# Kernel tuning notes

Hardware: AMD Instinct MI355X
Metric: run time of the kernel (lower is better)

The kernel has to match this reference:

```python
import jax, jax.numpy as jnp
import numpy as np

# ---- Cl(4,1) geometric-product Cayley table: gp(a,b)[k] = a[i] b[j] C[i,j,k] ----
def _build_cayley():
    metric = np.array([1.0, 1.0, 1.0, 1.0, -1.0], dtype=np.float32)  # signature (4,1)
    C = np.zeros((32, 32, 32), dtype=np.float32)
    for a in range(32):
        for b in range(32):
            # canonical reordering sign (count of swaps to merge blades)
            cnt = 0
            ash = a >> 1
            while ash:
                cnt += bin(ash & b).count('1')
                ash >>= 1
            s = -1.0 if (cnt & 1) else 1.0
            common = a & b
            for i in range(5):
                if (common >> i) & 1:
                    s *= metric[i]
            C[a, b, a ^ b] = s
    return C

CAYLEY = _build_cayley()
N_HEADS = 8

def gp_cl41(a, b, C):
    # a, b: (..., 32) multivectors
    return jnp.einsum('...i,...j,ijk->...k', a, b, C)

def normalize_cl41(x, eps=1e-6):
    n = jnp.sqrt(jnp.sum(x * x, axis=-1, keepdims=True) + eps)
    return x / n

def vlinear(x, w, b):
    # x: (..., Din, 32), w: (Dout, Din), b: (Dout, 32) -- blade-wise channel mixing
    return jnp.einsum('...ik,oi->...ok', x, w) + b

def layernorm2d(x, w, b, eps=1e-5):
    # normalized_shape = [D, 32]
    m = jnp.mean(x, axis=(-2, -1), keepdims=True)
    v = jnp.var(x, axis=(-2, -1), keepdims=True)
    return (x - m) / jnp.sqrt(v + eps) * w + b

def attention(x, wq, bq, wk, bk, wv, bv, wo, bo):
    B, S, D, K = x.shape
    hd = D // N_HEADS
    q = vlinear(x, wq, bq).reshape(B, S, N_HEADS, hd, K)
    k = vlinear(x, wk, bk).reshape(B, S, N_HEADS, hd, K)
    v = vlinear(x, wv, bv).reshape(B, S, N_HEADS, hd, K)
    scores = jnp.einsum('bqhdk,bshdk->bhqs', q, k) / jnp.sqrt(jnp.float32(hd * K))
    p = jax.nn.softmax(scores, axis=-1)
    o = jnp.einsum('bhqs,bshdk->bqhdk', p, v).reshape(B, S, D, K)
    return vlinear(o, wo, bo)


def setup_inputs() -> dict:
    key = jax.random.key(0)
    B, S, D, K = 4, 512, 256, 32
    L, E, NC = 2, 4, 1000
    ks = jax.random.split(key, 24)
    s = 1.0 / np.sqrt(D)
    inp = {
        'x': jax.random.normal(ks[0], (B, S, D, K), jnp.float32),
        'ln1_w': jnp.ones((L, D, K), jnp.float32),
        'ln1_b': jnp.zeros((L, D, K), jnp.float32),
        'wq': jax.random.normal(ks[1], (L, D, D), jnp.float32) * s,
        'bq': jnp.zeros((L, D, K), jnp.float32),
        'wk': jax.random.normal(ks[2], (L, D, D), jnp.float32) * s,
        'bk': jnp.zeros((L, D, K), jnp.float32),
        'wv': jax.random.normal(ks[3], (L, D, D), jnp.float32) * s,
        'bv': jnp.zeros((L, D, K), jnp.float32),
        'wo': jax.random.normal(ks[4], (L, D, D), jnp.float32) * s,
        'bo': jnp.zeros((L, D, K), jnp.float32),
        'ln2_w': jnp.ones((L, D, K), jnp.float32),
        'ln2_b': jnp.zeros((L, D, K), jnp.float32),
        'w1': jax.random.normal(ks[5], (L, E * D, D), jnp.float32) * s,
        'b1': jnp.zeros((L, E * D, K), jnp.float32),
        'w2': jax.random.normal(ks[6], (L, D, E * D), jnp.float32) * (1.0 / np.sqrt(E * D)),
        'b2': jnp.zeros((L, D, K), jnp.float32),
        'wr': jax.random.normal(ks[7], (D, D), jnp.float32) * s,
        'br': jnp.zeros((D, K), jnp.float32),
        'wc': jax.random.normal(ks[8], (NC, D * K), jnp.float32) * 0.02,
        'bc': jnp.zeros((NC,), jnp.float32),
    }
    return inp


def reference(x, ln1_w, ln1_b, wq, bq, wk, bk, wv, bv, wo, bo,
              ln2_w, ln2_b, w1, b1, w2, b2, wr, br, wc, bc):
    C = jnp.asarray(CAYLEY)
    L = ln1_w.shape[0]
    for l in range(L):
        h = layernorm2d(x, ln1_w[l], ln1_b[l])
        x = x + attention(h, wq[l], bq[l], wk[l], bk[l], wv[l], bv[l], wo[l], bo[l])
        x = normalize_cl41(x)
        h = layernorm2d(x, ln2_w[l], ln2_b[l])
        h = jnp.tanh(vlinear(h, w1[l], b1[l]))
        x = x + vlinear(h, w2[l], b2[l])
        x = normalize_cl41(x)
    # Recursive Rotor Accumulator pooling: psi_{t+1} = normalize(gp(r_t, psi_t))
    delta = vlinear(x, wr, br)                    # (B, S, D, 32)
    B, S, D, K = delta.shape
    psi0 = jnp.zeros((B, D, K), x.dtype).at[..., 0].set(1.0)
    def step(psi, r_t):
        return normalize_cl41(gp_cl41(r_t, psi, C)), None
    psi, _ = jax.lax.scan(step, psi0, jnp.moveaxis(delta, 1, 0))
    logits = psi.reshape(B, D * K) @ wc.T + bc
    return logits
```

## Files before the change

kernel.cpp:

```cpp
#include <hip/hip_runtime.h>
#include <hip/hip_bf16.h>
#include <cstdint>
#include <cstddef>

typedef __bf16 bf16_t;
typedef __attribute__((ext_vector_type(8))) __bf16 bf16x8;
typedef __attribute__((ext_vector_type(4))) __bf16 bf16x4;
typedef __attribute__((ext_vector_type(4))) float f32x4;

#define DEV __device__ __forceinline__

DEV void async16(const bf16_t* g, bf16_t* l) {
  __builtin_amdgcn_global_load_lds((const __attribute__((address_space(1))) void*)g,
                                   (__attribute__((address_space(3))) void*)l, 16, 0, 0);
}

DEV float fast_tanh(float x) {
  const float ex = __expf(2.f * x);
  return 1.f - 2.f / (ex + 1.f);
}

enum { EPI_RESID = 0, EPI_FFN1 = 1, EPI_QKV = 2, EPI_SCORE = 3, EPI_PV = 4, EPI_DELTAT = 5 };

template<int EPI, bool TRANSB>
__global__ __launch_bounds__(256, 2)
void gemm_k(const bf16_t* __restrict__ A, const bf16_t* __restrict__ A2,
            const bf16_t* __restrict__ B, const bf16_t* __restrict__ B2,
            const float* __restrict__ bias, void* __restrict__ outp, void* __restrict__ outp2,
            int Kd, int lda, int ldb, long aStride, long bStride)
{
  __shared__ bf16_t sA [2][4096];
  __shared__ bf16_t sB [2][4096];
  __shared__ bf16_t sA2[2][4096];
  __shared__ bf16_t sB2[2][4096];

  const int tid  = threadIdx.x;
  const int lane = tid & 63;
  const int wv   = tid >> 6;
  const int wr   = wv >> 1, wc = wv & 1;

  unsigned gx = gridDim.x, gy = gridDim.y;
  unsigned nb = gx * gy * gridDim.z;
  unsigned fid = blockIdx.x + gx * (blockIdx.y + gy * blockIdx.z);
  if ((nb & 7u) == 0u) fid = (fid & 7u) * (nb >> 3) + (fid >> 3);
  const unsigned bxu = fid % gx;
  const unsigned rem = fid / gx;
  const unsigned byu = rem % gy;
  const unsigned bzu = rem / gy;
  const int m0 = byu * 128;
  const int n0 = bxu * 128;
  const int bz = bzu;

  const bf16_t *Ab, *Bb, *A2b, *B2b;
  if constexpr (EPI == EPI_SCORE) {
    const int h = bz & 7;
    const long ho = (long)(bz >> 3) * 512;
    Ab  = A  + (long)h * aStride + ho;
    Bb  = B  + (long)h * bStride + ho;
    A2b = A2 + (long)h * aStride + ho;
    B2b = B2 + (long)h * bStride + ho;
  } else {
    Ab  = A  + (long)bz * aStride;
    Bb  = B  + (long)bz * bStride;
    A2b = A2 + (long)bz * aStride;
    B2b = B2 + (long)bz * bStride;
  }

  const int sRow = tid >> 2;
  const int sKo  = (tid & 3) * 8;
  const int tr = tid & 15;
  const int tc = tid >> 4;

  f32x4 acc[4][4];
#pragma unroll
  for (int i = 0; i < 4; i++)
#pragma unroll
    for (int j = 0; j < 4; j++) acc[i][j] = f32x4{0.f, 0.f, 0.f, 0.f};

  const int ns  = Kd >> 5;
  const int off = (int)(fid & (unsigned)(ns - 1));

  uint4 br0, br1, br2, br3;

  auto stageA = [&](int si, int b) {
    const int kt = ((si + off) & (ns - 1)) << 5;
    const bf16_t* ga  = Ab  + (long)(m0 + sRow) * lda + kt + sKo;
    const bf16_t* ga2 = A2b + (long)(m0 + sRow) * lda + kt + sKo;
    async16(ga,             &sA [b][tid * 8]);
    async16(ga + 64 * lda,  &sA [b][2048 + tid * 8]);
    async16(ga2,            &sA2[b][tid * 8]);
    async16(ga2 + 64 * lda, &sA2[b][2048 + tid * 8]);
  };
  auto stageB = [&](int si, int b) {
    const int kt = ((si + off) & (ns - 1)) << 5;
    const bf16_t* gb  = Bb  + (long)(n0 + sRow) * ldb + kt + sKo;
    const bf16_t* gb2 = B2b + (long)(n0 + sRow) * ldb + kt + sKo;
    async16(gb,             &sB [b][tid * 8]);
    async16(gb + 64 * ldb,  &sB [b][2048 + tid * 8]);
    async16(gb2,            &sB2[b][tid * 8]);
    async16(gb2 + 64 * ldb, &sB2[b][2048 + tid * 8]);
  };
  auto loadBR = [&](int si) {
    const int kt = ((si + off) & (ns - 1)) << 5;
    const bf16_t* gb  = Bb  + (long)(kt + tr) * ldb + n0 + tc * 8;
    const bf16_t* gb2 = B2b + (long)(kt + tr) * ldb + n0 + tc * 8;
    br0 = *(const uint4*)gb;
    br1 = *(const uint4*)(gb + 16 * ldb);
    br2 = *(const uint4*)gb2;
    br3 = *(const uint4*)(gb2 + 16 * ldb);
  };

  stageA(0, 0);
  if constexpr (!TRANSB) stageB(0, 0); else loadBR(0);

  for (int si = 0; si < ns; si++) {
    const int cb = si & 1;
    if (si + 1 < ns) stageA(si + 1, cb ^ 1);
    if constexpr (TRANSB) {
      const bf16_t* e0 = (const bf16_t*)&br0;
      const bf16_t* e1 = (const bf16_t*)&br1;
      const bf16_t* e2 = (const bf16_t*)&br2;
      const bf16_t* e3 = (const bf16_t*)&br3;
#pragma unroll
      for (int j = 0; j < 8; j++) {
        sB [cb][(tc * 8 + j) * 32 + tr]      = e0[j];
        sB [cb][(tc * 8 + j) * 32 + tr + 16] = e1[j];
        sB2[cb][(tc * 8 + j) * 32 + tr]      = e2[j];
        sB2[cb][(tc * 8 + j) * 32 + tr + 16] = e3[j];
      }
      if (si + 1 < ns) loadBR(si + 1);
      if (si + 1 >= ns) asm volatile("s_waitcnt vmcnt(0)" ::: "memory");
    } else {
      if (si + 1 < ns) {
        stageB(si + 1, cb ^ 1);
        asm volatile("s_waitcnt vmcnt(8)" ::: "memory");
      } else {
        asm volatile("s_waitcnt vmcnt(0)" ::: "memory");
      }
    }
    __syncthreads();

    bf16x8 af[4], bfr[4], af2[4], bf2[4];
#pragma unroll
    for (int i = 0; i < 4; i++) {
      const int ao = (wr * 64 + i * 16 + (lane & 15)) * 32 + (lane >> 4) * 8;
      const int bo = (wc * 64 + i * 16 + (lane & 15)) * 32 + (lane >> 4) * 8;
      af[i]  = *(const bf16x8*)&sA [cb][ao];
      af2[i] = *(const bf16x8*)&sA2[cb][ao];
      bfr[i] = *(const bf16x8*)&sB [cb][bo];
      bf2[i] = *(const bf16x8*)&sB2[cb][bo];
    }
#pragma unroll
    for (int i = 0; i < 4; i++)
#pragma unroll
      for (int j = 0; j < 4; j++) {
        acc[i][j] = __builtin_amdgcn_mfma_f32_16x16x32_bf16(af[i],  bfr[j], acc[i][j], 0, 0, 0);
        acc[i][j] = __builtin_amdgcn_mfma_f32_16x16x32_bf16(af[i],  bf2[j], acc[i][j], 0, 0, 0);
        acc[i][j] = __builtin_amdgcn_mfma_f32_16x16x32_bf16(af2[i], bfr[j], acc[i][j], 0, 0, 0);
      }
    __syncthreads();
  }

  const int cn = lane & 15;
  const int rg = (lane >> 4) * 4;
#pragma unroll
  for (int i = 0; i < 4; i++) {
    const int mb = m0 + wr * 64 + i * 16 + rg;
#pragma unroll
    for (int j = 0; j < 4; j++) {
      const int n = n0 + wc * 64 + j * 16 + cn;
#pragma unroll
      for (int r = 0; r < 4; r++) {
        const int m = mb + r;
        const float v = acc[i][j][r];
        if constexpr (EPI == EPI_RESID) {
          const float bb = bias ? bias[n * 32 + (m & 31)] : 0.f;
          ((float*)outp)[(long)m * 256 + n] += v + bb;
        } else if constexpr (EPI == EPI_QKV) {
          const int s = m >> 5, kb = m & 31;
          const int proj = n >> 8, col = n & 255;
          const int h = col >> 5, dd = col & 31;
          const long oidx = (long)proj * 4194304 + (long)(h * 512 + s) * 1024 + kb * 32 + dd;
          const float t = v + bias[n * 32 + kb];
          const bf16_t hh = (bf16_t)t;
          ((bf16_t*)outp)[oidx]  = hh;
          ((bf16_t*)outp2)[oidx] = (bf16_t)(t - (float)hh);
        } else if constexpr (EPI == EPI_SCORE) {
          const int h = bz & 7, half = bz >> 3;
          float* dst = half ? (float*)outp2 : (float*)outp;
          dst[(long)h * 262144 + (long)m * 512 + n] = v * (1.f / 32.f);
        } else if constexpr (EPI == EPI_PV) {
          const int kb = n >> 5, dd = n & 31;
          const long oidx = (long)(m * 32 + kb) * 256 + bz * 32 + dd;
          const bf16_t hh = (bf16_t)v;
          ((bf16_t*)outp)[oidx]  = hh;
          ((bf16_t*)outp2)[oidx] = (bf16_t)(v - (float)hh);
        } else {
          const int b = m >> 14, t = (m >> 5) & 511, kb = m & 31;
          ((float*)outp)[(((long)(b * 256 + n) * 512 + t) * 32) + kb] = v + bias[n * 32 + kb];
        }
      }
    }
  }
}

__global__ __launch_bounds__(512, 1)
void ffn_k(const bf16_t* __restrict__ Ah, const bf16_t* __restrict__ Al,
           const bf16_t* __restrict__ W1h_, const bf16_t* __restrict__ W1l_,
           const bf16_t* __restrict__ W2h_, const bf16_t* __restrict__ W2l_,
           const float* __restrict__ b1, const float* __restrict__ b2,
           float* __restrict__ XT)
{
  __shared__ bf16_t sAh[64 * 256], sAl[64 * 256];
  __shared__ bf16_t sWh[8192], sWl[8192];
  __shared__ bf16_t sHh[64 * 136], sHl[64 * 136];

  const int tid  = threadIdx.x;
  const int lane = tid & 63;
  const int wv   = tid >> 6;
  const int wm   = wv >> 2;
  const int wn   = wv & 3;
  const int l15  = lane & 15;
  const int lg   = lane >> 4;
  const int m0   = blockIdx.x * 64;
  const int coff = blockIdx.x & 7;
  const int soff = (blockIdx.x >> 3) & 7;
  const int toff = (blockIdx.x >> 3) & 3;

#pragma unroll
  for (int r = 0; r < 4; r++) {
    const int idx = r * 512 + tid;
    const int row = idx >> 5, cp = idx & 31;
    const int c = cp ^ (row & 31);
    async16(Ah + (long)(m0 + row) * 256 + c * 8, sAh + idx * 8);
    async16(Al + (long)(m0 + row) * 256 + c * 8, sAl + idx * 8);
  }
  asm volatile("s_waitcnt vmcnt(0)" ::: "memory");
  __syncthreads();

  f32x4 acc2[2][4];
#pragma unroll
  for (int i = 0; i < 2; i++)
#pragma unroll
    for (int j = 0; j < 4; j++) acc2[i][j] = f32x4{0.f, 0.f, 0.f, 0.f};

  const int wrow = tid >> 2;
  const int wc1  = (tid & 3) ^ (wrow & 3);

#pragma unroll 1
  for (int cc = 0; cc < 8; cc++) {
    const int ch = (cc + coff) & 7;
    const bf16_t* W1h = W1h_ + (long)(ch * 128) * 256;
    const bf16_t* W1l = W1l_ + (long)(ch * 128) * 256;
    async16(W1h + (long)wrow * 256 + soff * 32 + wc1 * 8, sWh + tid * 8);
    async16(W1l + (long)wrow * 256 + soff * 32 + wc1 * 8, sWl + tid * 8);

    f32x4 acc1[2][2];
#pragma unroll
    for (int i = 0; i < 2; i++)
#pragma unroll
      for (int j = 0; j < 2; j++) acc1[i][j] = f32x4{0.f, 0.f, 0.f, 0.f};

    for (int s = 0; s < 8; s++) {
      const int cb = (s & 1) * 4096;
      const int sp = (s + soff) & 7;
      if (s < 7) {
        const int nbuf = ((s + 1) & 1) * 4096;
        const int spn = (s + 1 + soff) & 7;
        async16(W1h + (long)wrow * 256 + spn * 32 + wc1 * 8, sWh + nbuf + tid * 8);
        async16(W1l + (long)wrow * 256 + spn * 32 + wc1 * 8, sWl + nbuf + tid * 8);
        asm volatile("s_waitcnt vmcnt(2)" ::: "memory");
      } else {
        asm volatile("s_waitcnt vmcnt(0)" ::: "memory");
      }
      __syncthreads();
      bf16x8 a_h[2], a_l[2], w_h[2], w_l[2];
#pragma unroll
      for (int i = 0; i < 2; i++) {
        const int arow = wm * 32 + i * 16 + l15;
        const int ac = (sp * 4 + lg) ^ (arow & 31);
        a_h[i] = *(const bf16x8*)&sAh[arow * 256 + ac * 8];
        a_l[i] = *(const bf16x8*)&sAl[arow * 256 + ac * 8];
      }
#pragma unroll
      for (int j = 0; j < 2; j++) {
        const int nrow = wn * 32 + j * 16 + l15;
        const int ncp = lg ^ (nrow & 3);
        w_h[j] = *(const bf16x8*)&sWh[cb + nrow * 32 + ncp * 8];
        w_l[j] = *(const bf16x8*)&sWl[cb + nrow * 32 + ncp * 8];
      }
#pragma unroll
      for (int i = 0; i < 2; i++)
#pragma unroll
        for (int j = 0; j < 2; j++) {
          acc1[i][j] = __builtin_amdgcn_mfma_f32_16x16x32_bf16(w_h[j], a_h[i], acc1[i][j], 0, 0, 0);
          acc1[i][j] = __builtin_amdgcn_mfma_f32_16x16x32_bf16(w_h[j], a_l[i], acc1[i][j], 0, 0, 0);
          acc1[i][j] = __builtin_amdgcn_mfma_f32_16x16x32_bf16(w_l[j], a_h[i], acc1[i][j], 0, 0, 0);
        }
      __syncthreads();
    }

    uint4 wrg_h[2], wrg_l[2];
#pragma unroll
    for (int r = 0; r < 2; r++) {
      const int idx = r * 512 + tid;
      const int row = idx >> 2;
      const int c = (idx & 3) ^ (row & 3);
      wrg_h[r] = *(const uint4*)(W2h_ + (long)row * 1024 + ch * 128 + toff * 32 + c * 8);
      wrg_l[r] = *(const uint4*)(W2l_ + (long)row * 1024 + ch * 128 + toff * 32 + c * 8);
    }

#pragma unroll
    for (int i = 0; i < 2; i++) {
      const int m = wm * 32 + i * 16 + l15;
      const int kb = (m0 + m) & 31;
#pragma unroll
      for (int j = 0; j < 2; j++) {
        const int nb4 = wn * 32 + j * 16 + lg * 4;
        bf16x4 h4, l4;
#pragma unroll
        for (int rr = 0; rr < 4; rr++) {
          const int n = nb4 + rr;
          const float t = fast_tanh(acc1[i][j][rr] + b1[(ch * 128 + n) * 32 + kb]);
          const bf16_t hh = (bf16_t)t;
          h4[rr] = hh;
          l4[rr] = (bf16_t)(t - (float)hh);
        }
        *(bf16x4*)&sHh[m * 136 + nb4] = h4;
        *(bf16x4*)&sHl[m * 136 + nb4] = l4;
      }
    }
    __syncthreads();

    for (int t = 0; t < 4; t++) {
      const int tp = (t + toff) & 3;
#pragma unroll
      for (int r = 0; r < 2; r++) {
        const int idx = r * 512 + tid;
        *(uint4*)&sWh[idx * 8] = wrg_h[r];
        *(uint4*)&sWl[idx * 8] = wrg_l[r];
      }
      __syncthreads();
      if (t < 3) {
        const int tpn = (t + 1 + toff) & 3;
#pragma unroll
        for (int r = 0; r < 2; r++) {
          const int idx = r * 512 + tid;
          const int row = idx >> 2;
          const int c = (idx & 3) ^ (row & 3);
          wrg_h[r] = *(const uint4*)(W2h_ + (long)row * 1024 + ch * 128 + tpn * 32 + c * 8);
          wrg_l[r] = *(const uint4*)(W2l_ + (long)row * 1024 + ch * 128 + tpn * 32 + c * 8);
        }
      }
      bf16x8 h_h[2], h_l[2], v_h[4], v_l[4];
#pragma unroll
      for (int i = 0; i < 2; i++) {
        const int hrow = wm * 32 + i * 16 + l15;
        h_h[i] = *(const bf16x8*)&sHh[hrow * 136 + tp * 32 + lg * 8];
        h_l[i] = *(const bf16x8*)&sHl[hrow * 136 + tp * 32 + lg * 8];
      }
#pragma unroll
      for (int j = 0; j < 4; j++) {
        const int n2 = wn * 64 + j * 16 + l15;
        const int ncp = lg ^ (n2 & 3);
        v_h[j] = *(const bf16x8*)&sWh[n2 * 32 + ncp * 8];
        v_l[j] = *(const bf16x8*)&sWl[n2 * 32 + ncp * 8];
      }
#pragma unroll
      for (int i = 0; i < 2; i++)
#pragma unroll
        for (int j = 0; j < 4; j++) {
          acc2[i][j] = __builtin_amdgcn_mfma_f32_16x16x32_bf16(h_h[i], v_h[j], acc2[i][j], 0, 0, 0);
          acc2[i][j] = __builtin_amdgcn_mfma_f32_16x16x32_bf16(h_h[i], v_l[j], acc2[i][j], 0, 0, 0);
          acc2[i][j] = __builtin_amdgcn_mfma_f32_16x16x32_bf16(h_l[i], v_h[j], acc2[i][j], 0, 0, 0);
        }
      __syncthreads();
    }
  }

#pragma unroll
  for (int i = 0; i < 2; i++)
#pragma unroll
    for (int j = 0; j < 4; j++) {
      const int n2 = wn * 64 + j * 16 + l15;
#pragma unroll
      for (int rr = 0; rr < 4; rr++) {
        const int m = m0 + wm * 32 + i * 16 + lg * 4 + rr;
        XT[(long)m * 256 + n2] += acc2[i][j][rr] + b2[n2 * 32 + (m & 31)];
      }
    }
}

__global__ __launch_bounds__(256)
void transpose_k(const float* __restrict__ src, float* __restrict__ dst, int R, int C)
{
  __shared__ float t[32][33];
  const long boff = (long)blockIdx.z * R * C;
  const int r0 = blockIdx.y * 32, c0 = blockIdx.x * 32;
  const int tx = threadIdx.x & 31, ty = threadIdx.x >> 5;
#pragma unroll
  for (int i = 0; i < 32; i += 8)
    t[ty + i][tx] = src[boff + (long)(r0 + ty + i) * C + c0 + tx];
  __syncthreads();
#pragma unroll
  for (int i = 0; i < 32; i += 8)
    dst[boff + (long)(c0 + ty + i) * R + r0 + tx] = t[tx][ty + i];
}

DEV void hilo4(const f32x4 t, bf16x4& h, bf16x4& l) {
#pragma unroll
  for (int j = 0; j < 4; j++) {
    const bf16_t hh = (bf16_t)t[j];
    h[j] = hh;
    l[j] = (bf16_t)(t[j] - (float)hh);
  }
}

template<int MODE>
__global__ __launch_bounds__(256)
void nl_k(const float* __restrict__ X, float* __restrict__ Xo,
          const float* __restrict__ wT, const float* __restrict__ bT,
          bf16_t* __restrict__ oh, bf16_t* __restrict__ ol)
{
  const int row = blockIdx.x * 4 + (threadIdx.x >> 6);
  const int l   = threadIdx.x & 63;
  const float4* Xr = (const float4*)X + (long)row * 2048 + l;
  f32x4 v[32];
#pragma unroll
  for (int kb = 0; kb < 32; kb++) {
    const float4 t = Xr[kb * 64];
    v[kb] = f32x4{t.x, t.y, t.z, t.w};
  }
  if constexpr (MODE & 1) {
    f32x4 ss = f32x4{1e-6f, 1e-6f, 1e-6f, 1e-6f};
#pragma unroll
    for (int kb = 0; kb < 32; kb++) ss += v[kb] * v[kb];
    const f32x4 rs = f32x4{rsqrtf(ss[0]), rsqrtf(ss[1]), rsqrtf(ss[2]), rsqrtf(ss[3])};
#pragma unroll
    for (int kb = 0; kb < 32; kb++) v[kb] *= rs;
    if constexpr (MODE & 2) {
      float4* Xw = (float4*)Xo + (long)row * 2048 + l;
#pragma unroll
      for (int kb = 0; kb < 32; kb++)
        Xw[kb * 64] = float4{v[kb][0], v[kb][1], v[kb][2], v[kb][3]};
    }
  }
  if constexpr (MODE & 4) {
    float s = 0.f, s2 = 0.f;
#pragma unroll
    for (int kb = 0; kb < 32; kb++) {
      s  += (v[kb][0] + v[kb][1]) + (v[kb][2] + v[kb][3]);
      s2 += (v[kb][0] * v[kb][0] + v[kb][1] * v[kb][1]) +
            (v[kb][2] * v[kb][2] + v[kb][3] * v[kb][3]);
    }
#pragma unroll
    for (int o = 32; o > 0; o >>= 1) { s += __shfl_xor(s, o); s2 += __shfl_xor(s2, o); }
    const float mean = s * (1.f / 8192.f);
    const float var  = s2 * (1.f / 8192.f) - mean * mean;
    const float rstd = rsqrtf(var + 1e-5f);
    const float4* w4 = (const float4*)wT + l;
    const float4* b4 = (const float4*)bT + l;
#pragma unroll
    for (int kb = 0; kb < 32; kb++) {
      const float4 ww = w4[kb * 64];
      const float4 bb = b4[kb * 64];
      f32x4 t;
      t[0] = (v[kb][0] - mean) * rstd * ww.x + bb.x;
      t[1] = (v[kb][1] - mean) * rstd * ww.y + bb.y;
      t[2] = (v[kb][2] - mean) * rstd * ww.z + bb.z;
      t[3] = (v[kb][3] - mean) * rstd * ww.w + bb.w;
      bf16x4 h4, l4;
      hilo4(t, h4, l4);
      const long oi = (long)row * 8192 + kb * 256 + l * 4;
      *(bf16x4*)&oh[oi] = h4;
      *(bf16x4*)&ol[oi] = l4;
    }
  }
  if constexpr (MODE & 8) {
#pragma unroll
    for (int kb = 0; kb < 32; kb++) {
      bf16x4 h4, l4;
      hilo4(v[kb], h4, l4);
      const long oi = (long)row * 8192 + kb * 256 + l * 4;
      *(bf16x4*)&oh[oi] = h4;
      *(bf16x4*)&ol[oi] = l4;
    }
  }
}

__global__ __launch_bounds__(256)
void softmax_k(const float* __restrict__ SC, const float* __restrict__ SC2,
               bf16_t* __restrict__ Ph, bf16_t* __restrict__ Pl)
{
  const int row = blockIdx.x * 4 + (threadIdx.x >> 6);
  const int lane = threadIdx.x & 63;
  const float* s1 = SC  + (long)row * 512;
  const float* s2 = SC2 + (long)row * 512;
  float4 a = *(const float4*)&s1[lane * 4];
  float4 c = *(const float4*)&s1[256 + lane * 4];
  const float4 a2 = *(const float4*)&s2[lane * 4];
  const float4 c2 = *(const float4*)&s2[256 + lane * 4];
  a.x += a2.x; a.y += a2.y; a.z += a2.z; a.w += a2.w;
  c.x += c2.x; c.y += c2.y; c.z += c2.z; c.w += c2.w;
  float mx = fmaxf(fmaxf(fmaxf(a.x, a.y), fmaxf(a.z, a.w)),
                   fmaxf(fmaxf(c.x, c.y), fmaxf(c.z, c.w)));
#pragma unroll
  for (int o = 32; o > 0; o >>= 1) mx = fmaxf(mx, __shfl_xor(mx, o));
  float e[8] = {expf(a.x - mx), expf(a.y - mx), expf(a.z - mx), expf(a.w - mx),
                expf(c.x - mx), expf(c.y - mx), expf(c.z - mx), expf(c.w - mx)};
  float sum = ((e[0] + e[1]) + (e[2] + e[3])) + ((e[4] + e[5]) + (e[6] + e[7]));
#pragma unroll
  for (int o = 32; o > 0; o >>= 1) sum += __shfl_xor(sum, o);
  const float inv = 1.f / sum;
  bf16x4 h0, h1, l0, l1;
#pragma unroll
  for (int j = 0; j < 4; j++) {
    const float p0 = e[j] * inv, p1 = e[4 + j] * inv;
    h0[j] = (bf16_t)p0; l0[j] = (bf16_t)(p0 - (float)h0[j]);
    h1[j] = (bf16_t)p1; l1[j] = (bf16_t)(p1 - (float)h1[j]);
  }
  *(bf16x4*)&Ph[(long)row * 512 + lane * 4] = h0;
  *(bf16x4*)&Ph[(long)row * 512 + 256 + lane * 4] = h1;
  *(bf16x4*)&Pl[(long)row * 512 + lane * 4] = l0;
  *(bf16x4*)&Pl[(long)row * 512 + 256 + lane * 4] = l1;
}

constexpr float gpsign(int i, int j) {
  int cnt = 0;
  for (int s = 1; s < 5; s++) cnt += __builtin_popcount((i >> s) & j);
  float sgn = (cnt & 1) ? -1.f : 1.f;
  if ((i & j) & 16) sgn = -sgn;
  return sgn;
}

DEV void gp32(const float* __restrict__ a, const float* __restrict__ b, float* __restrict__ o) {
#pragma unroll
  for (int k = 0; k < 32; k++) {
    float s0 = 0.f, s1 = 0.f;
#pragma unroll
    for (int i = 0; i < 32; i += 2) {
      s0 = fmaf(gpsign(i, i ^ k) * a[i], b[i ^ k], s0);
      s1 = fmaf(gpsign(i + 1, (i + 1) ^ k) * a[i + 1], b[(i + 1) ^ k], s1);
    }
    o[k] = s0 + s1;
  }
}

__global__ __launch_bounds__(256)
void gptree_k(const float* __restrict__ dT, float* __restrict__ psiO)
{
  __shared__ float bufA[256 * 33];
  __shared__ float bufB[128 * 33];
  const int chain = blockIdx.x;
  const int t = threadIdx.x;
  const float* src = dT + (long)chain * (512 * 32);
  {
    float v[64];
    const float4* g = (const float4*)(src + t * 64);
#pragma unroll
    for (int i = 0; i < 16; i++) *(float4*)&v[i * 4] = g[i];
    float o[32];
    gp32(v + 32, v, o);
    float ss = 1e-6f;
#pragma unroll
    for (int k = 0; k < 32; k++) ss = fmaf(o[k], o[k], ss);
    const float rs = rsqrtf(ss);
#pragma unroll
    for (int k = 0; k < 32; k++) bufA[t * 33 + k] = o[k] * rs;
  }
  __syncthreads();
  int cur = 0;
#pragma unroll 1
  for (int P = 128; P >= 1; P >>= 1) {
    const float* in = cur ? bufB : bufA;
    float* ob = cur ? bufA : bufB;
    if (t < P) {
      float a[32], b[32], o[32];
#pragma unroll
      for (int c = 0; c < 32; c++) { b[c] = in[t * 66 + c]; a[c] = in[t * 66 + 33 + c]; }
      gp32(a, b, o);
      float ss = 1e-6f;
#pragma unroll
      for (int k = 0; k < 32; k++) ss = fmaf(o[k], o[k], ss);
      const float rs = rsqrtf(ss);
#pragma unroll
      for (int k = 0; k < 32; k++) ob[t * 33 + k] = o[k] * rs;
    }
    cur ^= 1;
    __syncthreads();
  }
  if (t < 32) psiO[(long)chain * 32 + t] = (cur ? bufB : bufA)[t];
}

__global__ __launch_bounds__(256)
void cls_k(const float* __restrict__ psi, const float* __restrict__ wcw,
           const float* __restrict__ bc, float* __restrict__ out)
{
  const int c = blockIdx.x;
  const int tid = threadIdx.x;
  float a0 = 0.f, a1 = 0.f, a2 = 0.f, a3 = 0.f;
  for (int i = tid * 4; i < 8192; i += 1024) {
    const float4 w  = *(const float4*)&wcw[(long)c * 8192 + i];
    const float4 p0 = *(const float4*)&psi[i];
    const float4 p1 = *(const float4*)&psi[8192 + i];
    const float4 p2 = *(const float4*)&psi[16384 + i];
    const float4 p3 = *(const float4*)&psi[24576 + i];
    a0 += w.x * p0.x + w.y * p0.y + w.z * p0.z + w.w * p0.w;
    a1 += w.x * p1.x + w.y * p1.y + w.z * p1.z + w.w * p1.w;
    a2 += w.x * p2.x + w.y * p2.y + w.z * p2.z + w.w * p2.w;
    a3 += w.x * p3.x + w.y * p3.y + w.z * p3.z + w.w * p3.w;
  }
#pragma unroll
  for (int o = 32; o > 0; o >>= 1) {
    a0 += __shfl_down(a0, o); a1 += __shfl_down(a1, o);
    a2 += __shfl_down(a2, o); a3 += __shfl_down(a3, o);
  }
  __shared__ float red[4][4];
  const int wv = tid >> 6;
  if ((tid & 63) == 0) { red[wv][0] = a0; red[wv][1] = a1; red[wv][2] = a2; red[wv][3] = a3; }
  __syncthreads();
  if (tid < 4) {
    const float r = red[0][tid] + red[1][tid] + red[2][tid] + red[3][tid] + bc[c];
    out[(long)tid * 1000 + c] = r;
  }
}

__global__ void split_k(const float* __restrict__ in, bf16_t* __restrict__ h,
                        bf16_t* __restrict__ l, int n)
{
  const int i = blockIdx.x * 256 + threadIdx.x;
  if (i < n) {
    const float v = in[i];
    const bf16_t hh = (bf16_t)v;
    h[i] = hh;
    l[i] = (bf16_t)(v - (float)hh);
  }
}

__global__ void cpy_k(const float* __restrict__ in, float* __restrict__ o, int n)
{
  const int i = blockIdx.x * 256 + threadIdx.x;
  if (i < n) o[i] = in[i];
}

extern "C" void kernel_launch(void* const* d_in, const int* in_sizes, int n_in,
                              void* d_out, int out_size, void* d_ws, size_t ws_size,
                              hipStream_t stream)
{
  const float* x    = (const float*)d_in[0];
  const float* ln1w = (const float*)d_in[1];
  const float* ln1b = (const float*)d_in[2];
  const float* wq   = (const float*)d_in[3];
  const float* bq   = (const float*)d_in[4];
  const float* wk   = (const float*)d_in[5];
  const float* bk   = (const float*)d_in[6];
  const float* wvv  = (const float*)d_in[7];
  const float* bv   = (const float*)d_in[8];
  const float* wo   = (const float*)d_in[9];
  const float* bo   = (const float*)d_in[10];
  const float* ln2w = (const float*)d_in[11];
  const float* ln2b = (const float*)d_in[12];
  const float* w1   = (const float*)d_in[13];
  const float* b1   = (const float*)d_in[14];
  const float* w2   = (const float*)d_in[15];
  const float* b2   = (const float*)d_in[16];
  const float* wr   = (const float*)d_in[17];
  const float* br   = (const float*)d_in[18];
  const float* wcw  = (const float*)d_in[19];
  const float* bc   = (const float*)d_in[20];
  float* out = (float*)d_out;

  char* ws = (char*)d_ws;
  const size_t MB = 1ull << 20;
  const size_t KB = 1024;
  float*  XT   = (float*)(ws + 0);
  bf16_t* HBh  = (bf16_t*)(ws + 64 * MB);
  bf16_t* HBl  = (bf16_t*)(ws + 96 * MB);
  bf16_t* QKVh = (bf16_t*)(ws + 128 * MB);
  bf16_t* QKVl = (bf16_t*)(ws + 152 * MB);
  float*  SCb  = (float*)(ws + 176 * MB);
  float*  SC2b = (float*)(ws + 184 * MB);
  bf16_t* Ph   = QKVh;
  bf16_t* Pl   = QKVl;
  bf16_t* OBh  = QKVh + 4194304;
  bf16_t* OBl  = QKVl + 4194304;
  bf16_t* Vh   = QKVh + 8388608;
  bf16_t* Vl   = QKVl + 8388608;
  bf16_t* XHI = (bf16_t*)(ws + 64 * MB), *XLO = (bf16_t*)(ws + 96 * MB);
  float*  DELTAT = (float*)(ws + 128 * MB);
  float*  PSI  = (float*)(ws + 192 * MB);
  char*   W    = ws + 193 * MB;
  bf16_t* WQKVh = (bf16_t*)(W);
  bf16_t* WQKVl = (bf16_t*)(W + 1 * MB);
  bf16_t* W1h = (bf16_t*)(W + 2 * MB);   bf16_t* W1l = (bf16_t*)(W + 3 * MB);
  bf16_t* W2h = (bf16_t*)(W + 4 * MB);   bf16_t* W2l = (bf16_t*)(W + 5 * MB);
  bf16_t* WOh = (bf16_t*)(W + 6 * MB);   bf16_t* WOl = (bf16_t*)(W + 6 * MB + 256 * KB);
  bf16_t* WRh = (bf16_t*)(W + 6 * MB + 512 * KB);
  bf16_t* WRl = (bf16_t*)(W + 6 * MB + 640 * KB);
  float*  BQKV = (float*)(W + 6 * MB + 768 * KB);
  float*  LNT  = (float*)(W + 6 * MB + 960 * KB);
  float* LN1WT = LNT, *LN1BT = LNT + 16384, *LN2WT = LNT + 32768, *LN2BT = LNT + 49152;

  for (int l = 0; l < 2; l++) {
    split_k<<<256, 256, 0, stream>>>(wq + l * 65536, WQKVh + l * 196608, WQKVl + l * 196608, 65536);
    split_k<<<256, 256, 0, stream>>>(wk + l * 65536, WQKVh + l * 196608 + 65536, WQKVl + l * 196608 + 65536, 65536);
    split_k<<<256, 256, 0, stream>>>(wvv + l * 65536, WQKVh + l * 196608 + 131072, WQKVl + l * 196608 + 131072, 65536);
    cpy_k<<<32, 256, 0, stream>>>(bq + l * 8192, BQKV + l * 24576, 8192);
    cpy_k<<<32, 256, 0, stream>>>(bk + l * 8192, BQKV + l * 24576 + 8192, 8192);
    cpy_k<<<32, 256, 0, stream>>>(bv + l * 8192, BQKV + l * 24576 + 16384, 8192);
  }
  split_k<<<512, 256, 0, stream>>>(wo, WOh, WOl, 131072);
  split_k<<<2048, 256, 0, stream>>>(w1, W1h, W1l, 524288);
  split_k<<<2048, 256, 0, stream>>>(w2, W2h, W2l, 524288);
  split_k<<<256, 256, 0, stream>>>(wr, WRh, WRl, 65536);
  transpose_k<<<dim3(1, 8, 2), 256, 0, stream>>>(ln1w, LN1WT, 256, 32);
  transpose_k<<<dim3(1, 8, 2), 256, 0, stream>>>(ln1b, LN1BT, 256, 32);
  transpose_k<<<dim3(1, 8, 2), 256, 0, stream>>>(ln2w, LN2WT, 256, 32);
  transpose_k<<<dim3(1, 8, 2), 256, 0, stream>>>(ln2b, LN2BT, 256, 32);

  transpose_k<<<dim3(1, 8, 2048), 256, 0, stream>>>(x, XT, 256, 32);

  for (int l = 0; l < 2; l++) {
    if (l == 0)
      nl_k<4><<<512, 256, 0, stream>>>(XT, nullptr, LN1WT, LN1BT, HBh, HBl);
    for (int b = 0; b < 4; b++) {
      const long ao = (long)b * 16384 * 256;
      gemm_k<EPI_QKV, false><<<dim3(6, 128, 1), 256, 0, stream>>>(
          HBh + ao, HBl + ao, WQKVh + l * 196608, WQKVl + l * 196608,
          BQKV + l * 24576, QKVh, QKVl, 256, 256, 256, 0, 0);
      gemm_k<EPI_SCORE, false><<<dim3(4, 4, 16), 256, 0, stream>>>(
          QKVh, QKVl, QKVh + 4194304, QKVl + 4194304,
          nullptr, SCb, SC2b, 512, 1024, 1024, 512 * 1024, 512 * 1024);
      softmax_k<<<1024, 256, 0, stream>>>(SCb, SC2b, Ph, Pl);
      gemm_k<EPI_PV, true><<<dim3(8, 4, 8), 256, 0, stream>>>(
          Ph, Pl, Vh, Vl, nullptr, OBh, OBl, 512, 512, 1024, 512 * 512, 512 * 1024);
      gemm_k<EPI_RESID, false><<<dim3(2, 128, 1), 256, 0, stream>>>(
          OBh, OBl, WOh + l * 65536, WOl + l * 65536,
          bo + l * 8192, (float*)XT + ao, nullptr, 256, 256, 256, 0, 0);
    }
    nl_k<1 | 2 | 4><<<512, 256, 0, stream>>>(XT, XT, LN2WT + l * 8192, LN2BT + l * 8192, HBh, HBl);
    ffn_k<<<1024, 512, 0, stream>>>(HBh, HBl,
                                    W1h + l * 262144, W1l + l * 262144,
                                    W2h + l * 262144, W2l + l * 262144,
                                    b1 + l * 32768, b2 + l * 8192, XT);
    if (l == 0) {
      nl_k<1 | 2 | 4><<<512, 256, 0, stream>>>(XT, XT, LN1WT + 8192, LN1BT + 8192, HBh, HBl);
    } else {
      nl_k<1 | 8><<<512, 256, 0, stream>>>(XT, nullptr, nullptr, nullptr, XHI, XLO);
    }
  }

  gemm_k<EPI_DELTAT, false><<<dim3(2, 512, 1), 256, 0, stream>>>(
      XHI, XLO, WRh, WRl, br, DELTAT, nullptr, 256, 256, 256, 0, 0);
  gptree_k<<<1024, 256, 0, stream>>>(DELTAT, PSI);
  cls_k<<<1000, 256, 0, stream>>>(PSI, wcw, bc, out);
}
```

Measured before the change: 2.158 ms.

## Halve FFN row tile to 32 rows for two blocks per CU

The fused FFN kernel now processes 32 rows per block instead of 64, doubling the grid and roughly halving LDS and accumulator registers so two 512-thread blocks can be resident per CU. The hidden-activation buffer drops its padded stride of 136 in favour of an XOR-swizzled stride of 128 to avoid bank conflicts while saving LDS. In exchange, each block reuses every loaded W1/W2 tile across only half as many rows, which doubles the weight traffic from L2 and lowers the MFMA count per sync.

```diff
diff --git a/kernel.cpp b/kernel.cpp
--- a/kernel.cpp
+++ b/kernel.cpp
@@ -204,16 +204,16 @@
   }
 }
 
-__global__ __launch_bounds__(512, 1)
+__global__ __launch_bounds__(512, 2)
 void ffn_k(const bf16_t* __restrict__ Ah, const bf16_t* __restrict__ Al,
            const bf16_t* __restrict__ W1h_, const bf16_t* __restrict__ W1l_,
            const bf16_t* __restrict__ W2h_, const bf16_t* __restrict__ W2l_,
            const float* __restrict__ b1, const float* __restrict__ b2,
            float* __restrict__ XT)
 {
-  __shared__ bf16_t sAh[64 * 256], sAl[64 * 256];
+  __shared__ bf16_t sAh[32 * 256], sAl[32 * 256];
   __shared__ bf16_t sWh[8192], sWl[8192];
-  __shared__ bf16_t sHh[64 * 136], sHl[64 * 136];
+  __shared__ bf16_t sHh[32 * 128], sHl[32 * 128];
 
   const int tid  = threadIdx.x;
   const int lane = tid & 63;
@@ -222,13 +222,13 @@
   const int wn   = wv & 3;
   const int l15  = lane & 15;
   const int lg   = lane >> 4;
-  const int m0   = blockIdx.x * 64;
+  const int m0   = blockIdx.x * 32;
   const int coff = blockIdx.x & 7;
   const int soff = (blockIdx.x >> 3) & 7;
   const int toff = (blockIdx.x >> 3) & 3;
 
 #pragma unroll
-  for (int r = 0; r < 4; r++) {
+  for (int r = 0; r < 2; r++) {
     const int idx = r * 512 + tid;
     const int row = idx >> 5, cp = idx & 31;
     const int c = cp ^ (row & 31);
@@ -238,11 +238,9 @@
   asm volatile("s_waitcnt vmcnt(0)" ::: "memory");
   __syncthreads();
 
-  f32x4 acc2[2][4];
-#pragma unroll
-  for (int i = 0; i < 2; i++)
-#pragma unroll
-    for (int j = 0; j < 4; j++) acc2[i][j] = f32x4{0.f, 0.f, 0.f, 0.f};
+  f32x4 acc2[4];
+#pragma unroll
+  for (int j = 0; j < 4; j++) acc2[j] = f32x4{0.f, 0.f, 0.f, 0.f};
 
   const int wrow = tid >> 2;
   const int wc1  = (tid & 3) ^ (wrow & 3);
@@ -255,11 +253,9 @@
     async16(W1h + (long)wrow * 256 + soff * 32 + wc1 * 8, sWh + tid * 8);
     async16(W1l + (long)wrow * 256 + soff * 32 + wc1 * 8, sWl + tid * 8);
 
-    f32x4 acc1[2][2];
-#pragma unroll
-    for (int i = 0; i < 2; i++)
-#pragma unroll
-      for (int j = 0; j < 2; j++) acc1[i][j] = f32x4{0.f, 0.f, 0.f, 0.f};
+    f32x4 acc1[2];
+#pragma unroll
+    for (int j = 0; j < 2; j++) acc1[j] = f32x4{0.f, 0.f, 0.f, 0.f};
 
     for (int s = 0; s < 8; s++) {
       const int cb = (s & 1) * 4096;
@@ -274,13 +270,12 @@
         asm volatile("s_waitcnt vmcnt(0)" ::: "memory");
       }
       __syncthreads();
-      bf16x8 a_h[2], a_l[2], w_h[2], w_l[2];
-#pragma unroll
-      for (int i = 0; i < 2; i++) {
-        const int arow = wm * 32 + i * 16 + l15;
+      bf16x8 a_h, a_l, w_h[2], w_l[2];
+      {
+        const int arow = wm * 16 + l15;
         const int ac = (sp * 4 + lg) ^ (arow & 31);
-        a_h[i] = *(const bf16x8*)&sAh[arow * 256 + ac * 8];
-        a_l[i] = *(const bf16x8*)&sAl[arow * 256 + ac * 8];
+        a_h = *(const bf16x8*)&sAh[arow * 256 + ac * 8];
+        a_l = *(const bf16x8*)&sAl[arow * 256 + ac * 8];
       }
 #pragma unroll
       for (int j = 0; j < 2; j++) {
@@ -290,13 +285,11 @@
         w_l[j] = *(const bf16x8*)&sWl[cb + nrow * 32 + ncp * 8];
       }
 #pragma unroll
-      for (int i = 0; i < 2; i++)
-#pragma unroll
-        for (int j = 0; j < 2; j++) {
-          acc1[i][j] = __builtin_amdgcn_mfma_f32_16x16x32_bf16(w_h[j], a_h[i], acc1[i][j], 0, 0, 0);
-          acc1[i][j] = __builtin_amdgcn_mfma_f32_16x16x32_bf16(w_h[j], a_l[i], acc1[i][j], 0, 0, 0);
-          acc1[i][j] = __builtin_amdgcn_mfma_f32_16x16x32_bf16(w_l[j], a_h[i], acc1[i][j], 0, 0, 0);
-        }
+      for (int j = 0; j < 2; j++) {
+        acc1[j] = __builtin_amdgcn_mfma_f32_16x16x32_bf16(w_h[j], a_h, acc1[j], 0, 0, 0);
+        acc1[j] = __builtin_amdgcn_mfma_f32_16x16x32_bf16(w_h[j], a_l, acc1[j], 0, 0, 0);
+        acc1[j] = __builtin_amdgcn_mfma_f32_16x16x32_bf16(w_l[j], a_h, acc1[j], 0, 0, 0);
+      }
       __syncthreads();
     }
 
@@ -310,24 +303,25 @@
       wrg_l[r] = *(const uint4*)(W2l_ + (long)row * 1024 + ch * 128 + toff * 32 + c * 8);
     }
 
-#pragma unroll
-    for (int i = 0; i < 2; i++) {
-      const int m = wm * 32 + i * 16 + l15;
+    {
+      const int m = wm * 16 + l15;
       const int kb = (m0 + m) & 31;
 #pragma unroll
       for (int j = 0; j < 2; j++) {
-        const int nb4 = wn * 32 + j * 16 + lg * 4;
+        const int u = wn * 4 + j * 2 + (lg >> 1);
+        const int pu = u ^ (m & 7);
+        const int base = m * 128 + pu * 8 + (lg & 1) * 4;
+        const int ncol = wn * 32 + j * 16 + lg * 4;
         bf16x4 h4, l4;
 #pragma unroll
         for (int rr = 0; rr < 4; rr++) {
-          const int n = nb4 + rr;
-          const float t = fast_tanh(acc1[i][j][rr] + b1[(ch * 128 + n) * 32 + kb]);
+          const float t = fast_tanh(acc1[j][rr] + b1[(ch * 128 + ncol + rr) * 32 + kb]);
           const bf16_t hh = (bf16_t)t;
           h4[rr] = hh;
           l4[rr] = (bf16_t)(t - (float)hh);
         }
-        *(bf16x4*)&sHh[m * 136 + nb4] = h4;
-        *(bf16x4*)&sHl[m * 136 + nb4] = l4;
+        *(bf16x4*)&sHh[base] = h4;
+        *(bf16x4*)&sHl[base] = l4;
       }
     }
     __syncthreads();
@@ -352,12 +346,12 @@
           wrg_l[r] = *(const uint4*)(W2l_ + (long)row * 1024 + ch * 128 + tpn * 32 + c * 8);
         }
       }
-      bf16x8 h_h[2], h_l[2], v_h[4], v_l[4];
-#pragma unroll
-      for (int i = 0; i < 2; i++) {
-        const int hrow = wm * 32 + i * 16 + l15;
-        h_h[i] = *(const bf16x8*)&sHh[hrow * 136 + tp * 32 + lg * 8];
-        h_l[i] = *(const bf16x8*)&sHl[hrow * 136 + tp * 32 + lg * 8];
+      bf16x8 h_h, h_l, v_h[4], v_l[4];
+      {
+        const int hrow = wm * 16 + l15;
+        const int pu = (tp * 4 + lg) ^ (hrow & 7);
+        h_h = *(const bf16x8*)&sHh[hrow * 128 + pu * 8];
+        h_l = *(const bf16x8*)&sHl[hrow * 128 + pu * 8];
       }
 #pragma unroll
       for (int j = 0; j < 4; j++) {
@@ -367,28 +361,24 @@
         v_l[j] = *(const bf16x8*)&sWl[n2 * 32 + ncp * 8];
       }
 #pragma unroll
-      for (int i = 0; i < 2; i++)
-#pragma unroll
-        for (int j = 0; j < 4; j++) {
-          acc2[i][j] = __builtin_amdgcn_mfma_f32_16x16x32_bf16(h_h[i], v_h[j], acc2[i][j], 0, 0, 0);
-          acc2[i][j] = __builtin_amdgcn_mfma_f32_16x16x32_bf16(h_h[i], v_l[j], acc2[i][j], 0, 0, 0);
-          acc2[i][j] = __builtin_amdgcn_mfma_f32_16x16x32_bf16(h_l[i], v_h[j], acc2[i][j], 0, 0, 0);
-        }
+      for (int j = 0; j < 4; j++) {
+        acc2[j] = __builtin_amdgcn_mfma_f32_16x16x32_bf16(h_h, v_h[j], acc2[j], 0, 0, 0);
+        acc2[j] = __builtin_amdgcn_mfma_f32_16x16x32_bf16(h_h, v_l[j], acc2[j], 0, 0, 0);
+        acc2[j] = __builtin_amdgcn_mfma_f32_16x16x32_bf16(h_l, v_h[j], acc2[j], 0, 0, 0);
+      }
       __syncthreads();
     }
   }
 
 #pragma unroll
-  for (int i = 0; i < 2; i++)
-#pragma unroll
-    for (int j = 0; j < 4; j++) {
-      const int n2 = wn * 64 + j * 16 + l15;
-#pragma unroll
-      for (int rr = 0; rr < 4; rr++) {
-        const int m = m0 + wm * 32 + i * 16 + lg * 4 + rr;
-        XT[(long)m * 256 + n2] += acc2[i][j][rr] + b2[n2 * 32 + (m & 31)];
-      }
-    }
+  for (int j = 0; j < 4; j++) {
+    const int n2 = wn * 64 + j * 16 + l15;
+#pragma unroll
+    for (int rr = 0; rr < 4; rr++) {
+      const int m = m0 + wm * 16 + lg * 4 + rr;
+      XT[(long)m * 256 + n2] += acc2[j][rr] + b2[n2 * 32 + (m & 31)];
+    }
+  }
 }
 
 __global__ __launch_bounds__(256)
@@ -739,7 +729,7 @@
           bo + l * 8192, (float*)XT + ao, nullptr, 256, 256, 256, 0, 0);
     }
     nl_k<1 | 2 | 4><<<512, 256, 0, stream>>>(XT, XT, LN2WT + l * 8192, LN2BT + l * 8192, HBh, HBl);
-    ffn_k<<<1024, 512, 0, stream>>>(HBh, HBl,
+    ffn_k<<<2048, 512, 0, stream>>>(HBh, HBl,
                                     W1h + l * 262144, W1l + l * 262144,
                                     W2h + l * 262144, W2l + l * 262144,
                                     b1 + l * 32768, b2 + l * 8192, XT);
```

Result: slower. 2.830 ms (+31.1%).

## Shrink FFN tile to 32 rows and read weights directly from global

Applied to the files above, without the earlier changes.

The fused FFN kernel now uses 256-thread blocks covering 32 rows each, launched as 2048 blocks with two blocks per CU. The LDS staging and double buffering of W1 and W2 tiles, with their barriers, are removed. Each wave now loads its weight fragments straight from global memory, relying on L1/L2 caching. This cuts LDS use and synchronisation and may raise occupancy, but weight traffic per row of output doubles, and the uncoalesced per-lane global loads sit right before the MFMAs with no prefetch to hide their latency.

```diff
diff --git a/kernel.cpp b/kernel.cpp
--- a/kernel.cpp
+++ b/kernel.cpp
@@ -204,32 +204,29 @@
   }
 }
 
-__global__ __launch_bounds__(512, 1)
+__global__ __launch_bounds__(256, 2)
 void ffn_k(const bf16_t* __restrict__ Ah, const bf16_t* __restrict__ Al,
            const bf16_t* __restrict__ W1h_, const bf16_t* __restrict__ W1l_,
            const bf16_t* __restrict__ W2h_, const bf16_t* __restrict__ W2l_,
            const float* __restrict__ b1, const float* __restrict__ b2,
            float* __restrict__ XT)
 {
-  __shared__ bf16_t sAh[64 * 256], sAl[64 * 256];
-  __shared__ bf16_t sWh[8192], sWl[8192];
-  __shared__ bf16_t sHh[64 * 136], sHl[64 * 136];
+  __shared__ bf16_t sAh[32 * 256], sAl[32 * 256];
+  __shared__ bf16_t sHh[32 * 136], sHl[32 * 136];
 
   const int tid  = threadIdx.x;
   const int lane = tid & 63;
-  const int wv   = tid >> 6;
-  const int wm   = wv >> 2;
-  const int wn   = wv & 3;
+  const int wn   = tid >> 6;
   const int l15  = lane & 15;
   const int lg   = lane >> 4;
-  const int m0   = blockIdx.x * 64;
+  const int m0   = blockIdx.x * 32;
   const int coff = blockIdx.x & 7;
   const int soff = (blockIdx.x >> 3) & 7;
   const int toff = (blockIdx.x >> 3) & 3;
 
 #pragma unroll
   for (int r = 0; r < 4; r++) {
-    const int idx = r * 512 + tid;
+    const int idx = r * 256 + tid;
     const int row = idx >> 5, cp = idx & 31;
     const int c = cp ^ (row & 31);
     async16(Ah + (long)(m0 + row) * 256 + c * 8, sAh + idx * 8);
@@ -243,17 +240,12 @@
   for (int i = 0; i < 2; i++)
 #pragma unroll
     for (int j = 0; j < 4; j++) acc2[i][j] = f32x4{0.f, 0.f, 0.f, 0.f};
-
-  const int wrow = tid >> 2;
-  const int wc1  = (tid & 3) ^ (wrow & 3);
 
 #pragma unroll 1
   for (int cc = 0; cc < 8; cc++) {
     const int ch = (cc + coff) & 7;
     const bf16_t* W1h = W1h_ + (long)(ch * 128) * 256;
     const bf16_t* W1l = W1l_ + (long)(ch * 128) * 256;
-    async16(W1h + (long)wrow * 256 + soff * 32 + wc1 * 8, sWh + tid * 8);
-    async16(W1l + (long)wrow * 256 + soff * 32 + wc1 * 8, sWl + tid * 8);
 
     f32x4 acc1[2][2];
 #pragma unroll
@@ -261,23 +253,13 @@
 #pragma unroll
       for (int j = 0; j < 2; j++) acc1[i][j] = f32x4{0.f, 0.f, 0.f, 0.f};
 
+#pragma unroll 2
     for (int s = 0; s < 8; s++) {
-      const int cb = (s & 1) * 4096;
       const int sp = (s + soff) & 7;
-      if (s < 7) {
-        const int nbuf = ((s + 1) & 1) * 4096;
-        const int spn = (s + 1 + soff) & 7;
-        async16(W1h + (long)wrow * 256 + spn * 32 + wc1 * 8, sWh + nbuf + tid * 8);
-        async16(W1l + (long)wrow * 256 + spn * 32 + wc1 * 8, sWl + nbuf + tid * 8);
-        asm volatile("s_waitcnt vmcnt(2)" ::: "memory");
-      } else {
-        asm volatile("s_waitcnt vmcnt(0)" ::: "memory");
-      }
-      __syncthreads();
       bf16x8 a_h[2], a_l[2], w_h[2], w_l[2];
 #pragma unroll
       for (int i = 0; i < 2; i++) {
-        const int arow = wm * 32 + i * 16 + l15;
+        const int arow = i * 16 + l15;
         const int ac = (sp * 4 + lg) ^ (arow & 31);
         a_h[i] = *(const bf16x8*)&sAh[arow * 256 + ac * 8];
         a_l[i] = *(const bf16x8*)&sAl[arow * 256 + ac * 8];
@@ -285,9 +267,8 @@
 #pragma unroll
       for (int j = 0; j < 2; j++) {
         const int nrow = wn * 32 + j * 16 + l15;
-        const int ncp = lg ^ (nrow & 3);
-        w_h[j] = *(const bf16x8*)&sWh[cb + nrow * 32 + ncp * 8];
-        w_l[j] = *(const bf16x8*)&sWl[cb + nrow * 32 + ncp * 8];
+        w_h[j] = *(const bf16x8*)(W1h + (long)nrow * 256 + sp * 32 + lg * 8);
+        w_l[j] = *(const bf16x8*)(W1l + (long)nrow * 256 + sp * 32 + lg * 8);
       }
 #pragma unroll
       for (int i = 0; i < 2; i++)
@@ -297,22 +278,11 @@
           acc1[i][j] = __builtin_amdgcn_mfma_f32_16x16x32_bf16(w_h[j], a_l[i], acc1[i][j], 0, 0, 0);
           acc1[i][j] = __builtin_amdgcn_mfma_f32_16x16x32_bf16(w_l[j], a_h[i], acc1[i][j], 0, 0, 0);
         }
-      __syncthreads();
-    }
-
-    uint4 wrg_h[2], wrg_l[2];
-#pragma unroll
-    for (int r = 0; r < 2; r++) {
-      const int idx = r * 512 + tid;
-      const int row = idx >> 2;
-      const int c = (idx & 3) ^ (row & 3);
-      wrg_h[r] = *(const uint4*)(W2h_ + (long)row * 1024 + ch * 128 + toff * 32 + c * 8);
-      wrg_l[r] = *(const uint4*)(W2l_ + (long)row * 1024 + ch * 128 + toff * 32 + c * 8);
     }
 
 #pragma unroll
     for (int i = 0; i < 2; i++) {
-      const int m = wm * 32 + i * 16 + l15;
+      const int m = i * 16 + l15;
       const int kb = (m0 + m) & 31;
 #pragma unroll
       for (int j = 0; j < 2; j++) {
@@ -332,39 +302,21 @@
     }
     __syncthreads();
 
+#pragma unroll 2
     for (int t = 0; t < 4; t++) {
       const int tp = (t + toff) & 3;
-#pragma unroll
-      for (int r = 0; r < 2; r++) {
-        const int idx = r * 512 + tid;
-        *(uint4*)&sWh[idx * 8] = wrg_h[r];
-        *(uint4*)&sWl[idx * 8] = wrg_l[r];
-      }
-      __syncthreads();
-      if (t < 3) {
-        const int tpn = (t + 1 + toff) & 3;
-#pragma unroll
-        for (int r = 0; r < 2; r++) {
-          const int idx = r * 512 + tid;
-          const int row = idx >> 2;
-          const int c = (idx & 3) ^ (row & 3);
-          wrg_h[r] = *(const uint4*)(W2h_ + (long)row * 1024 + ch * 128 + tpn * 32 + c * 8);
-          wrg_l[r] = *(const uint4*)(W2l_ + (long)row * 1024 + ch * 128 + tpn * 32 + c * 8);
-        }
-      }
       bf16x8 h_h[2], h_l[2], v_h[4], v_l[4];
 #pragma unroll
       for (int i = 0; i < 2; i++) {
-        const int hrow = wm * 32 + i * 16 + l15;
+        const int hrow = i * 16 + l15;
         h_h[i] = *(const bf16x8*)&sHh[hrow * 136 + tp * 32 + lg * 8];
         h_l[i] = *(const bf16x8*)&sHl[hrow * 136 + tp * 32 + lg * 8];
       }
 #pragma unroll
       for (int j = 0; j < 4; j++) {
         const int n2 = wn * 64 + j * 16 + l15;
-        const int ncp = lg ^ (n2 & 3);
-        v_h[j] = *(const bf16x8*)&sWh[n2 * 32 + ncp * 8];
-        v_l[j] = *(const bf16x8*)&sWl[n2 * 32 + ncp * 8];
+        v_h[j] = *(const bf16x8*)(W2h_ + (long)n2 * 1024 + ch * 128 + tp * 32 + lg * 8);
+        v_l[j] = *(const bf16x8*)(W2l_ + (long)n2 * 1024 + ch * 128 + tp * 32 + lg * 8);
       }
 #pragma unroll
       for (int i = 0; i < 2; i++)
@@ -374,8 +326,8 @@
           acc2[i][j] = __builtin_amdgcn_mfma_f32_16x16x32_bf16(h_h[i], v_l[j], acc2[i][j], 0, 0, 0);
           acc2[i][j] = __builtin_amdgcn_mfma_f32_16x16x32_bf16(h_l[i], v_h[j], acc2[i][j], 0, 0, 0);
         }
-      __syncthreads();
-    }
+    }
+    __syncthreads();
   }
 
 #pragma unroll
@@ -385,7 +337,7 @@
       const int n2 = wn * 64 + j * 16 + l15;
 #pragma unroll
       for (int rr = 0; rr < 4; rr++) {
-        const int m = m0 + wm * 32 + i * 16 + lg * 4 + rr;
+        const int m = m0 + i * 16 + lg * 4 + rr;
         XT[(long)m * 256 + n2] += acc2[i][j][rr] + b2[n2 * 32 + (m & 31)];
       }
     }
@@ -739,7 +691,7 @@
           bo + l * 8192, (float*)XT + ao, nullptr, 256, 256, 256, 0, 0);
     }
     nl_k<1 | 2 | 4><<<512, 256, 0, stream>>>(XT, XT, LN2WT + l * 8192, LN2BT + l * 8192, HBh, HBl);
-    ffn_k<<<1024, 512, 0, stream>>>(HBh, HBl,
+    ffn_k<<<2048, 256, 0, stream>>>(HBh, HBl,
                                     W1h + l * 262144, W1l + l * 262144,
                                     W2h + l * 262144, W2l + l * 262144,
                                     b1 + l * 32768, b2 + l * 8192, XT);
```

Measured after the change: 2.295 ms. +6.4%, slower.
